# Kernel tuning notes

Hardware: AMD Instinct MI355X
Metric: run time of the kernel (lower is better)

The kernel has to match this reference:

```python
import jax, jax.numpy as jnp
import numpy as np
import math

INPUT_WIDTH = 1024
KEY_WIDTH = 64
VALUE_WIDTH = 64
NUM_HEADS = 16
NUM_GROUPS = 4
HEADS_PER_GROUP = NUM_HEADS // NUM_GROUPS  # w = 4


def setup_inputs() -> dict:
    key = jax.random.key(0)
    k_x, k_q, k_k, k_v, k_p = jax.random.split(key, 5)
    n, s = 2, 2048
    # torch.nn.Linear weights are [out, in]; we store transposed [in, out] for x @ W.
    def lin(k, fan_in, fan_out):
        bound = 1.0 / math.sqrt(fan_in)
        return jax.random.uniform(k, (fan_in, fan_out), minval=-bound, maxval=bound, dtype=jnp.float32)
    return {
        "X": jax.random.normal(k_x, (n, s, INPUT_WIDTH), dtype=jnp.float32),
        "Wq": lin(k_q, INPUT_WIDTH, NUM_HEADS * KEY_WIDTH),
        "Wk": lin(k_k, INPUT_WIDTH, NUM_GROUPS * KEY_WIDTH),
        "Wv": lin(k_v, INPUT_WIDTH, NUM_GROUPS * VALUE_WIDTH),
        "Wpost": lin(k_p, NUM_HEADS * VALUE_WIDTH, INPUT_WIDTH),
    }


def reference(X, Wq, Wk, Wv, Wpost):
    n, s, _ = X.shape
    # Projections (no bias)
    Q = (X @ Wq).reshape(n, s, NUM_GROUPS, HEADS_PER_GROUP, KEY_WIDTH)  # [b,s,g,w,e]
    K = (X @ Wk).reshape(n, s, NUM_GROUPS, KEY_WIDTH)                   # [b,t,g,e]
    V = (X @ Wv).reshape(n, s, NUM_GROUPS, VALUE_WIDTH)                 # [b,t,g,e]
    scale = 1.0 / math.sqrt(KEY_WIDTH)
    # Grouped cross-attention: scores [b,s,t,g,w]
    raw = jnp.einsum('bsgwe,btge->bstgw', Q, K * scale)
    attn = jax.nn.softmax(raw, axis=2)  # softmax over key positions t
    A = jnp.einsum('bstgw,btge->bsgwe', attn, V).reshape(n, s, NUM_HEADS * VALUE_WIDTH)
    P = A @ Wpost
    return X + P
```

## Files before the change

kernel.cpp:

```cpp
#include <hip/hip_runtime.h>
#include <hip/hip_bf16.h>
#include <hip/hip_fp16.h>
#include <math.h>

typedef __attribute__((ext_vector_type(8))) short bfrag8;
typedef __attribute__((ext_vector_type(8))) _Float16 hfrag8;
typedef __attribute__((ext_vector_type(4))) float facc4;
typedef __attribute__((ext_vector_type(16))) float facc16;

#define MFMA16B(a, b, c) __builtin_amdgcn_mfma_f32_16x16x32_bf16((a), (b), (c), 0, 0, 0)
#define MFMA32B(a, b, c) __builtin_amdgcn_mfma_f32_32x32x16_bf16((a), (b), (c), 0, 0, 0)
#define MFMA32H(a, b, c) __builtin_amdgcn_mfma_f32_32x32x16_f16((a), (b), (c), 0, 0, 0)

__device__ __forceinline__ void gload_lds16(const void* g, void* l) {
    __builtin_amdgcn_global_load_lds(
        (const __attribute__((address_space(1))) void*)g,
        (__attribute__((address_space(3))) void*)l, 16, 0, 0);
}

__device__ __forceinline__ unsigned short f2bf(float f) {
    unsigned u = __float_as_uint(f);
    u += 0x7fffu + ((u >> 16) & 1u);
    return (unsigned short)(u >> 16);
}

__device__ __forceinline__ unsigned pk2(float a, float b) {
    auto h = __builtin_amdgcn_cvt_pkrtz(a, b);
    union { decltype(h) h; unsigned u; } c;
    c.h = h;
    return c.u;
}

__device__ __forceinline__ void do_transpose(const float* __restrict__ src,
                                             unsigned short* __restrict__ dst,
                                             int Kdim, int N, int nb, int kb,
                                             float (*tile)[33], int tid) {
    int tx = tid & 31, ty = tid >> 5;
#pragma unroll
    for (int r = ty; r < 32; r += 8)
        tile[r][tx] = src[(size_t)(kb + r) * N + nb + tx];
    __syncthreads();
#pragma unroll
    for (int r = ty; r < 32; r += 8)
        dst[(size_t)(nb + r) * Kdim + kb + tx] = f2bf(tile[tx][r]);
}

__global__ __launch_bounds__(256) void k_prep(
    const float* __restrict__ X, const float* __restrict__ Wq,
    const float* __restrict__ Wk, const float* __restrict__ Wv,
    const float* __restrict__ Wp,
    unsigned short* __restrict__ Xb, unsigned short* __restrict__ Wqkvt,
    unsigned short* __restrict__ Wpt) {
    __shared__ float tile[32][33];
    int blk = blockIdx.x, tid = threadIdx.x;
    if (blk < 4096) {
        int i = (blk * 256 + tid) * 4;
        float4 v = *reinterpret_cast<const float4*>(X + i);
        unsigned short o[4] = {f2bf(v.x), f2bf(v.y), f2bf(v.z), f2bf(v.w)};
        *reinterpret_cast<ulonglong1*>(Xb + i) = *reinterpret_cast<ulonglong1*>(o);
    } else if (blk < 5120) {
        int idx = blk - 4096;
        do_transpose(Wq, Wqkvt, 1024, 1024, (idx & 31) * 32, (idx >> 5) * 32, tile, tid);
    } else if (blk < 5376) {
        int idx = blk - 5120;
        do_transpose(Wk, Wqkvt + 1024 * 1024, 1024, 256, (idx & 7) * 32, (idx >> 3) * 32, tile, tid);
    } else if (blk < 5632) {
        int idx = blk - 5376;
        do_transpose(Wv, Wqkvt + 1280 * 1024, 1024, 256, (idx & 7) * 32, (idx >> 3) * 32, tile, tid);
    } else {
        int idx = blk - 5632;
        do_transpose(Wp, Wpt, 1024, 1024, (idx & 31) * 32, (idx >> 5) * 32, tile, tid);
    }
}

template <int EPI>
__global__ __launch_bounds__(512) void k_gemm_bt(
    const unsigned short* __restrict__ A, const unsigned short* __restrict__ Bt,
    int M, int N, int K,
    unsigned short* __restrict__ Qo, unsigned short* __restrict__ Ko,
    unsigned short* __restrict__ Vto,
    const float* __restrict__ Xres, float* __restrict__ Out) {
    __shared__ char lds[49152];
    const int tid = threadIdx.x;
    const int lane = tid & 63, wid = tid >> 6;
    const int wr = wid >> 1, wc = wid & 1;
    const int l15 = lane & 15, lhi = lane >> 4;
    const int m0 = blockIdx.y * 128, n0 = blockIdx.x * 64;
    const int nk = K >> 6;

    facc4 acc[2][2] = {};

    auto STAGE = [&](int buf, int k0) {
#pragma unroll
        for (int i = 0; i < 2; ++i) {
            int p = (wid * 2 + i) * 1024 + lane * 16;
            int row = p >> 7;
            int src = (p & 127) ^ ((row & 7) << 4);
            gload_lds16(A + (size_t)(m0 + row) * K + k0 + (src >> 1),
                        lds + buf * 16384 + (wid * 2 + i) * 1024);
        }
        {
            int p = wid * 1024 + lane * 16;
            int row = p >> 7;
            int src = (p & 127) ^ ((row & 7) << 4);
            gload_lds16(Bt + (size_t)(n0 + row) * K + k0 + (src >> 1),
                        lds + 32768 + buf * 8192 + wid * 1024);
        }
    };

    STAGE(0, 0);
    __syncthreads();

    for (int t = 0; t < nk; ++t) {
        const int cur = t & 1;
        if (t + 1 < nk) STAGE(cur ^ 1, (t + 1) * 64);
        const char* Ab = lds + cur * 16384;
        const char* Bb = lds + 32768 + cur * 8192;
#pragma unroll
        for (int kc = 0; kc < 2; ++kc) {
            bfrag8 af[2], bfv[2];
#pragma unroll
            for (int mi = 0; mi < 2; ++mi) {
                int row = wr * 32 + mi * 16 + l15;
                int off = (row * 128 + kc * 64 + lhi * 16) ^ ((row & 7) << 4);
                af[mi] = *reinterpret_cast<const bfrag8*>(Ab + off);
            }
#pragma unroll
            for (int ni = 0; ni < 2; ++ni) {
                int row = wc * 32 + ni * 16 + l15;
                int off = (row * 128 + kc * 64 + lhi * 16) ^ ((row & 7) << 4);
                bfv[ni] = *reinterpret_cast<const bfrag8*>(Bb + off);
            }
#pragma unroll
            for (int mi = 0; mi < 2; ++mi)
#pragma unroll
                for (int ni = 0; ni < 2; ++ni)
                    acc[mi][ni] = MFMA16B(af[mi], bfv[ni], acc[mi][ni]);
        }
        __syncthreads();
    }

    if (EPI == 0 && n0 >= 1280) {
        unsigned short* VT = (unsigned short*)lds;
#pragma unroll
        for (int mi = 0; mi < 2; ++mi)
#pragma unroll
            for (int ni = 0; ni < 2; ++ni) {
                int col = wc * 32 + ni * 16 + l15;
                int row0 = wr * 32 + mi * 16 + lhi * 4;
                unsigned long long u = 0;
#pragma unroll
                for (int r = 0; r < 4; ++r)
                    u |= (unsigned long long)__half_as_ushort(__float2half(acc[mi][ni][r]))
                         << (16 * r);
                *reinterpret_cast<unsigned long long*>(VT + col * 136 + row0) = u;
            }
        __syncthreads();
        int c = tid >> 3, part = tid & 7;
        int b = m0 >> 11;
        int g = (n0 - 1280) >> 6;
        unsigned short* dstp =
            Vto + ((size_t)(b * 4 + g) * 64 + c) * 2048 + (m0 & 2047) + part * 16;
        const unsigned short* srcp = VT + c * 136 + part * 16;
        *(reinterpret_cast<uint4*>(dstp) + 0) = *(reinterpret_cast<const uint4*>(srcp) + 0);
        *(reinterpret_cast<uint4*>(dstp) + 1) = *(reinterpret_cast<const uint4*>(srcp) + 1);
        return;
    }

#pragma unroll
    for (int mi = 0; mi < 2; ++mi)
#pragma unroll
        for (int ni = 0; ni < 2; ++ni)
#pragma unroll
            for (int r = 0; r < 4; ++r) {
                int grow = m0 + wr * 32 + mi * 16 + lhi * 4 + r;
                int gcol = n0 + wc * 32 + ni * 16 + l15;
                float v = acc[mi][ni][r];
                if (EPI == 0) {
                    int b = grow >> 11, t = grow & 2047;
                    if (gcol < 1024) {
                        Qo[(size_t)grow * 1024 + gcol] = f2bf(v * 0.18033688f);
                    } else {
                        int cc = gcol - 1024;
                        int g = cc >> 6, e = cc & 63;
                        Ko[(((size_t)(b * 4 + g) * 2048 + t) << 6) + e] = f2bf(v);
                    }
                } else {
                    size_t idx = (size_t)grow * 1024 + gcol;
                    Out[idx] = Xres[idx] + v;
                }
            }
}

__global__ __launch_bounds__(512, 2) void k_attn(
    const unsigned short* __restrict__ Q,
    const unsigned short* __restrict__ Kb,
    const unsigned short* __restrict__ Vt,
    unsigned short* __restrict__ Abuf) {
    __shared__ char smem[49152];

    const int tid = threadIdx.x;
    const int lane = tid & 63, wid = tid >> 6;
    const int kvh = wid >> 2, qw = wid & 3;
    const int l31 = lane & 31, hi = lane >> 5;

    int wg = blockIdx.x;
    int swz = ((wg & 7) << 6) | (wg >> 3);
    const int qt = swz & 15, head = (swz >> 4) & 15, b = swz >> 8;
    const int g = head >> 2;
    const size_t kvK = (size_t)(b * 4 + g) * 2048 * 64;
    const size_t kvV = (size_t)(b * 4 + g) * 64 * 2048;
    const int qrow0 = b * 2048 + qt * 128 + qw * 32;

    bfrag8 qf[4];
#pragma unroll
    for (int ks = 0; ks < 4; ++ks)
        qf[ks] = *reinterpret_cast<const bfrag8*>(
            Q + (size_t)(qrow0 + l31) * 1024 + head * 64 + ks * 16 + hi * 8);

    const int p = qw * 1024 + lane * 16;
    const int rK = p >> 7;
    const int cK = (p & 127) ^ ((rK & 7) << 4);
    const unsigned short* srcK = Kb + kvK + (size_t)(kvh * 1024 + rK) * 64 + (cK >> 1);
    const int rV = p >> 6;
    const int cV = (p & 63) ^ ((rV & 6) << 3);
    const unsigned short* srcV = Vt + kvV + (size_t)rV * 2048 + kvh * 1024 + (cV >> 1);
    const int dK = kvh * 12288 + qw * 1024;
    const int dV = 24576 + kvh * 12288 + qw * 1024;

    facc16 o[2] = {};
    float psA = 0.f, psB = 0.f;

    gload_lds16(srcK, smem + dK);
    gload_lds16(srcV, smem + dV);
    gload_lds16(srcK + 32 * 64, smem + dK + 4096);
    gload_lds16(srcV + 32, smem + dV + 4096);

    for (int t = 0; t < 32; ++t) {
        if (t < 31) asm volatile("s_waitcnt vmcnt(2)" ::: "memory");
        else        asm volatile("s_waitcnt vmcnt(0)" ::: "memory");
        __builtin_amdgcn_s_barrier();
        __builtin_amdgcn_sched_barrier(0);
        if (t < 30) {
            const int bn = (t + 2) % 3;
            gload_lds16(srcK + (size_t)(t + 2) * (32 * 64), smem + dK + bn * 4096);
            gload_lds16(srcV + (size_t)(t + 2) * 32, smem + dV + bn * 4096);
        }
        const char* Kc = smem + kvh * 12288 + (t % 3) * 4096;
        const char* Vc = smem + 24576 + kvh * 12288 + (t % 3) * 4096;

        facc16 s = {};
        __builtin_amdgcn_s_setprio(1);
#pragma unroll
        for (int ks = 0; ks < 4; ++ks) {
            int off = (l31 * 128 + ks * 32 + hi * 16) ^ ((l31 & 7) << 4);
            bfrag8 kf = *reinterpret_cast<const bfrag8*>(Kc + off);
            s = MFMA32B(kf, qf[ks], s);
        }
        __builtin_amdgcn_s_setprio(0);

#pragma unroll
        for (int e = 0; e < 16; e += 2) {
            float e0 = __builtin_amdgcn_exp2f(s[e]);
            float e1 = __builtin_amdgcn_exp2f(s[e + 1]);
            s[e] = e0;
            s[e + 1] = e1;
            psA += e0;
            psB += e1;
        }
#pragma unroll
        for (int kh = 0; kh < 2; ++kh) {
            const int pb = kh * 2;
            unsigned a0 = pk2(s[4 * pb + 0], s[4 * pb + 1]);
            unsigned a1 = pk2(s[4 * pb + 2], s[4 * pb + 3]);
            unsigned b0 = pk2(s[4 * pb + 4], s[4 * pb + 5]);
            unsigned b1 = pk2(s[4 * pb + 6], s[4 * pb + 7]);
            asm("v_permlane32_swap_b32 %0, %1" : "+v"(a0), "+v"(b0));
            asm("v_permlane32_swap_b32 %0, %1" : "+v"(a1), "+v"(b1));
            union { unsigned u[4]; hfrag8 h; } pu;
            pu.u[0] = a0; pu.u[1] = a1; pu.u[2] = b0; pu.u[3] = b1;
            __builtin_amdgcn_s_setprio(1);
#pragma unroll
            for (int ot = 0; ot < 2; ++ot) {
                int row = ot * 32 + l31;
                int off = row * 64 + ((kh * 32 + hi * 16) ^ ((row & 6) << 3));
                hfrag8 vf = *reinterpret_cast<const hfrag8*>(Vc + off);
                o[ot] = MFMA32H(vf, pu.h, o[ot]);
            }
            __builtin_amdgcn_s_setprio(0);
        }
    }
    __syncthreads();

    float psum = psA + psB;
    float* cmO = (float*)smem;
    float* cmL = (float*)(smem + 32768);
    if (kvh == 1) {
#pragma unroll
        for (int ot = 0; ot < 2; ++ot)
#pragma unroll
            for (int r = 0; r < 16; ++r)
                cmO[qw * 2048 + (ot * 16 + r) * 64 + lane] = o[ot][r];
        cmL[qw * 64 + lane] = psum;
    }
    __syncthreads();
    if (kvh == 0) {
#pragma unroll
        for (int ot = 0; ot < 2; ++ot)
#pragma unroll
            for (int r = 0; r < 16; ++r)
                o[ot][r] += cmO[qw * 2048 + (ot * 16 + r) * 64 + lane];
        psum += cmL[qw * 64 + lane];

        float l = psum + __shfl_xor(psum, 32, 64);
        float rl = 1.0f / l;
        int arow = qrow0 + l31;
#pragma unroll
        for (int ot = 0; ot < 2; ++ot)
#pragma unroll
            for (int p2 = 0; p2 < 4; ++p2) {
                unsigned long long u = 0;
#pragma unroll
                for (int r = 0; r < 4; ++r)
                    u |= (unsigned long long)f2bf(o[ot][4 * p2 + r] * rl) << (16 * r);
                *reinterpret_cast<unsigned long long*>(
                    Abuf + (size_t)arow * 1024 + head * 64 + ot * 32 + p2 * 8 + hi * 4) = u;
            }
    }
}


extern "C" void kernel_launch(void* const* d_in, const int* in_sizes, int n_in,
                              void* d_out, int out_size, void* d_ws, size_t ws_size,
                              hipStream_t stream) {
    const float* X = (const float*)d_in[0];
    const float* Wq = (const float*)d_in[1];
    const float* Wk = (const float*)d_in[2];
    const float* Wv = (const float*)d_in[3];
    const float* Wpost = (const float*)d_in[4];
    float* Out = (float*)d_out;

    unsigned short* Xb = (unsigned short*)d_ws;
    unsigned short* Wqkvt = Xb + 4096 * 1024;
    unsigned short* Wpt = Wqkvt + 1536 * 1024;
    unsigned short* Qb = Wpt + 1024 * 1024;
    unsigned short* Kbuf = Qb + 4096 * 1024;
    unsigned short* Vtbuf = Kbuf + 8 * 2048 * 64;
    unsigned short* Abuf = Vtbuf + 8 * 2048 * 64;

    k_prep<<<6656, 256, 0, stream>>>(X, Wq, Wk, Wv, Wpost, Xb, Wqkvt, Wpt);

    k_gemm_bt<0><<<dim3(24, 32), 512, 0, stream>>>(Xb, Wqkvt, 4096, 1536, 1024,
                                                   Qb, Kbuf, Vtbuf, nullptr, nullptr);

    k_attn<<<512, 512, 0, stream>>>(Qb, Kbuf, Vtbuf, Abuf);

    k_gemm_bt<1><<<dim3(16, 32), 512, 0, stream>>>(Abuf, Wpt, 4096, 1024, 1024,
                                                   nullptr, nullptr, nullptr, X, Out);
}
```

Before: 89.43 us.

## Load V in 64-key tiles with double buffering and 128B swizzled rows

V^T tiles are now fetched as 64-key chunks (128-byte rows) every other iteration into a double buffer, instead of 32-key chunks each iteration in a triple buffer. K keeps its triple-buffered per-iteration pipeline, and the waitcnt values alternate to match the uneven issue pattern. The aim is longer contiguous global reads and fewer V load instructions. In exchange, LDS use grows and the prefetch distance for V changes. The QK accumulator is also initialised from a zero register rather than a fresh zero vector.

```diff
diff --git a/kernel.cpp b/kernel.cpp
--- a/kernel.cpp
+++ b/kernel.cpp
@@ -197,7 +197,7 @@
     const unsigned short* __restrict__ Kb,
     const unsigned short* __restrict__ Vt,
     unsigned short* __restrict__ Abuf) {
-    __shared__ char smem[49152];
+    __shared__ char smem[57344];
 
     const int tid = threadIdx.x;
     const int lane = tid & 63, wid = tid >> 6;
@@ -218,44 +218,58 @@
         qf[ks] = *reinterpret_cast<const bfrag8*>(
             Q + (size_t)(qrow0 + l31) * 1024 + head * 64 + ks * 16 + hi * 8);
 
-    const int p = qw * 1024 + lane * 16;
-    const int rK = p >> 7;
-    const int cK = (p & 127) ^ ((rK & 7) << 4);
-    const unsigned short* srcK = Kb + kvK + (size_t)(kvh * 1024 + rK) * 64 + (cK >> 1);
-    const int rV = p >> 6;
-    const int cV = (p & 63) ^ ((rV & 6) << 3);
-    const unsigned short* srcV = Vt + kvV + (size_t)rV * 2048 + kvh * 1024 + (cV >> 1);
+    const int pK = qw * 1024 + lane * 16;
+    const int rK = pK >> 7;
+    const int cKb = (pK & 127) ^ ((rK & 7) << 4);
+    const unsigned short* srcK = Kb + kvK + (size_t)(kvh * 1024 + rK) * 64 + (cKb >> 1);
     const int dK = kvh * 12288 + qw * 1024;
-    const int dV = 24576 + kvh * 12288 + qw * 1024;
+
+    const unsigned short* srcV[2];
+#pragma unroll
+    for (int j = 0; j < 2; ++j) {
+        int p = qw * 2048 + j * 1024 + lane * 16;
+        int rV = p >> 7;
+        int cVb = (p & 127) ^ ((rV & 7) << 4);
+        srcV[j] = Vt + kvV + (size_t)rV * 2048 + kvh * 1024 + (cVb >> 1);
+    }
+    const int dV0 = 24576 + kvh * 16384 + qw * 2048;
 
     facc16 o[2] = {};
+    facc16 fz = {};
     float psA = 0.f, psB = 0.f;
 
     gload_lds16(srcK, smem + dK);
-    gload_lds16(srcV, smem + dV);
+    gload_lds16(srcV[0], smem + dV0);
+    gload_lds16(srcV[1], smem + dV0 + 1024);
     gload_lds16(srcK + 32 * 64, smem + dK + 4096);
-    gload_lds16(srcV + 32, smem + dV + 4096);
 
     for (int t = 0; t < 32; ++t) {
-        if (t < 31) asm volatile("s_waitcnt vmcnt(2)" ::: "memory");
-        else        asm volatile("s_waitcnt vmcnt(0)" ::: "memory");
+        if (t == 31)      asm volatile("s_waitcnt vmcnt(0)" ::: "memory");
+        else if (t & 1)   asm volatile("s_waitcnt vmcnt(3)" ::: "memory");
+        else              asm volatile("s_waitcnt vmcnt(1)" ::: "memory");
         __builtin_amdgcn_s_barrier();
         __builtin_amdgcn_sched_barrier(0);
         if (t < 30) {
-            const int bn = (t + 2) % 3;
-            gload_lds16(srcK + (size_t)(t + 2) * (32 * 64), smem + dK + bn * 4096);
-            gload_lds16(srcV + (size_t)(t + 2) * 32, smem + dV + bn * 4096);
+            gload_lds16(srcK + (size_t)(t + 2) * (32 * 64),
+                        smem + dK + ((t + 2) % 3) * 4096);
+            if (!(t & 1)) {
+                int tv = (t >> 1) + 1;
+                int vb = (tv & 1) * 8192;
+                gload_lds16(srcV[0] + (size_t)tv * 64, smem + dV0 + vb);
+                gload_lds16(srcV[1] + (size_t)tv * 64, smem + dV0 + vb + 1024);
+            }
         }
         const char* Kc = smem + kvh * 12288 + (t % 3) * 4096;
-        const char* Vc = smem + 24576 + kvh * 12288 + (t % 3) * 4096;
-
-        facc16 s = {};
+        const char* Vc = smem + 24576 + kvh * 16384 + ((t >> 1) & 1) * 8192;
+        const int vcol = (t & 1) * 64;
+
+        facc16 s;
         __builtin_amdgcn_s_setprio(1);
 #pragma unroll
         for (int ks = 0; ks < 4; ++ks) {
             int off = (l31 * 128 + ks * 32 + hi * 16) ^ ((l31 & 7) << 4);
             bfrag8 kf = *reinterpret_cast<const bfrag8*>(Kc + off);
-            s = MFMA32B(kf, qf[ks], s);
+            s = MFMA32B(kf, qf[ks], ks == 0 ? fz : s);
         }
         __builtin_amdgcn_s_setprio(0);
 
@@ -283,8 +297,8 @@
 #pragma unroll
             for (int ot = 0; ot < 2; ++ot) {
                 int row = ot * 32 + l31;
-                int off = row * 64 + ((kh * 32 + hi * 16) ^ ((row & 6) << 3));
-                hfrag8 vf = *reinterpret_cast<const hfrag8*>(Vc + off);
+                int colb = (vcol + kh * 32 + hi * 16) ^ ((row & 7) << 4);
+                hfrag8 vf = *reinterpret_cast<const hfrag8*>(Vc + row * 128 + colb);
                 o[ot] = MFMA32H(vf, pu.h, o[ot]);
             }
             __builtin_amdgcn_s_setprio(0);
```

Result: no change. 90.75 us (+1.5%).

## Software-pipeline QK^T one tile ahead and use 4-stage LDS ring

Applied to the files above, without the earlier changes.

Computes the score MFMA for the next key tile before the exp/PV work of the current tile, so the exp2 VALU work can overlap with matrix-core work. The K/V LDS ring grows from 3 to 4 stages (48KB to 64KB shared memory), and prefetch loads are now issued before the barrier. The larger LDS footprint with launch bounds (512,2) may limit occupancy, and the extra live accumulator raises register pressure.

```diff
diff --git a/kernel.cpp b/kernel.cpp
--- a/kernel.cpp
+++ b/kernel.cpp
@@ -197,7 +197,7 @@
     const unsigned short* __restrict__ Kb,
     const unsigned short* __restrict__ Vt,
     unsigned short* __restrict__ Abuf) {
-    __shared__ char smem[49152];
+    __shared__ char smem[65536];
 
     const int tid = threadIdx.x;
     const int lane = tid & 63, wid = tid >> 6;
@@ -225,56 +225,73 @@
     const int rV = p >> 6;
     const int cV = (p & 63) ^ ((rV & 6) << 3);
     const unsigned short* srcV = Vt + kvV + (size_t)rV * 2048 + kvh * 1024 + (cV >> 1);
-    const int dK = kvh * 12288 + qw * 1024;
-    const int dV = 24576 + kvh * 12288 + qw * 1024;
+    const int dK = kvh * 16384 + qw * 1024;
+    const int dV = 32768 + kvh * 16384 + qw * 1024;
 
     facc16 o[2] = {};
+    const facc16 fz = {};
     float psA = 0.f, psB = 0.f;
 
     gload_lds16(srcK, smem + dK);
     gload_lds16(srcV, smem + dV);
     gload_lds16(srcK + 32 * 64, smem + dK + 4096);
     gload_lds16(srcV + 32, smem + dV + 4096);
+    asm volatile("s_waitcnt vmcnt(2)" ::: "memory");
+    __builtin_amdgcn_s_barrier();
+
+    facc16 scur;
+    {
+        const char* K0 = smem + kvh * 16384;
+#pragma unroll
+        for (int ks = 0; ks < 4; ++ks) {
+            int off = (l31 * 128 + ks * 32 + hi * 16) ^ ((l31 & 7) << 4);
+            bfrag8 kf = *reinterpret_cast<const bfrag8*>(K0 + off);
+            scur = MFMA32B(kf, qf[ks], ks == 0 ? fz : scur);
+        }
+    }
 
     for (int t = 0; t < 32; ++t) {
-        if (t < 31) asm volatile("s_waitcnt vmcnt(2)" ::: "memory");
-        else        asm volatile("s_waitcnt vmcnt(0)" ::: "memory");
+        if (t < 30) {
+            const int bn = (t + 2) & 3;
+            gload_lds16(srcK + (size_t)(t + 2) * (32 * 64), smem + dK + bn * 4096);
+            gload_lds16(srcV + (size_t)(t + 2) * 32, smem + dV + bn * 4096);
+            asm volatile("s_waitcnt vmcnt(2)" ::: "memory");
+        } else {
+            asm volatile("s_waitcnt vmcnt(0)" ::: "memory");
+        }
         __builtin_amdgcn_s_barrier();
         __builtin_amdgcn_sched_barrier(0);
-        if (t < 30) {
-            const int bn = (t + 2) % 3;
-            gload_lds16(srcK + (size_t)(t + 2) * (32 * 64), smem + dK + bn * 4096);
-            gload_lds16(srcV + (size_t)(t + 2) * 32, smem + dV + bn * 4096);
-        }
-        const char* Kc = smem + kvh * 12288 + (t % 3) * 4096;
-        const char* Vc = smem + 24576 + kvh * 12288 + (t % 3) * 4096;
-
-        facc16 s = {};
-        __builtin_amdgcn_s_setprio(1);
-#pragma unroll
-        for (int ks = 0; ks < 4; ++ks) {
-            int off = (l31 * 128 + ks * 32 + hi * 16) ^ ((l31 & 7) << 4);
-            bfrag8 kf = *reinterpret_cast<const bfrag8*>(Kc + off);
-            s = MFMA32B(kf, qf[ks], s);
-        }
-        __builtin_amdgcn_s_setprio(0);
-
+
+        facc16 snxt;
+        if (t < 31) {
+            const char* Kn = smem + kvh * 16384 + ((t + 1) & 3) * 4096;
+            __builtin_amdgcn_s_setprio(1);
+#pragma unroll
+            for (int ks = 0; ks < 4; ++ks) {
+                int off = (l31 * 128 + ks * 32 + hi * 16) ^ ((l31 & 7) << 4);
+                bfrag8 kf = *reinterpret_cast<const bfrag8*>(Kn + off);
+                snxt = MFMA32B(kf, qf[ks], ks == 0 ? fz : snxt);
+            }
+            __builtin_amdgcn_s_setprio(0);
+        }
+
+        const char* Vc = smem + 32768 + kvh * 16384 + (t & 3) * 4096;
 #pragma unroll
         for (int e = 0; e < 16; e += 2) {
-            float e0 = __builtin_amdgcn_exp2f(s[e]);
-            float e1 = __builtin_amdgcn_exp2f(s[e + 1]);
-            s[e] = e0;
-            s[e + 1] = e1;
+            float e0 = __builtin_amdgcn_exp2f(scur[e]);
+            float e1 = __builtin_amdgcn_exp2f(scur[e + 1]);
+            scur[e] = e0;
+            scur[e + 1] = e1;
             psA += e0;
             psB += e1;
         }
 #pragma unroll
         for (int kh = 0; kh < 2; ++kh) {
             const int pb = kh * 2;
-            unsigned a0 = pk2(s[4 * pb + 0], s[4 * pb + 1]);
-            unsigned a1 = pk2(s[4 * pb + 2], s[4 * pb + 3]);
-            unsigned b0 = pk2(s[4 * pb + 4], s[4 * pb + 5]);
-            unsigned b1 = pk2(s[4 * pb + 6], s[4 * pb + 7]);
+            unsigned a0 = pk2(scur[4 * pb + 0], scur[4 * pb + 1]);
+            unsigned a1 = pk2(scur[4 * pb + 2], scur[4 * pb + 3]);
+            unsigned b0 = pk2(scur[4 * pb + 4], scur[4 * pb + 5]);
+            unsigned b1 = pk2(scur[4 * pb + 6], scur[4 * pb + 7]);
             asm("v_permlane32_swap_b32 %0, %1" : "+v"(a0), "+v"(b0));
             asm("v_permlane32_swap_b32 %0, %1" : "+v"(a1), "+v"(b1));
             union { unsigned u[4]; hfrag8 h; } pu;
@@ -289,6 +306,7 @@
             }
             __builtin_amdgcn_s_setprio(0);
         }
+        scur = snxt;
     }
     __syncthreads();
 
```

Result: no change. 89.92 us (+0.6%).

## Load attention K/V fragments directly from global into registers, drop LDS staging

Applied to the files above, without the earlier changes.

The attention kernel no longer stages K and V tiles through LDS with async global-to-LDS loads and barriers. Each wave now reads its MFMA fragments straight from global memory, prefetching the next K tile one iteration ahead. Workgroups shrink from 512 to 256 threads (64 query rows instead of 128), with twice as many blocks. This removes the per-iteration barrier and LDS traffic, but K/V reuse across query waves now depends on L1/L2 caching, so global load traffic per wave goes up and V loads are not prefetched.

```diff
diff --git a/kernel.cpp b/kernel.cpp
--- a/kernel.cpp
+++ b/kernel.cpp
@@ -192,25 +192,25 @@
             }
 }
 
-__global__ __launch_bounds__(512, 2) void k_attn(
+__global__ __launch_bounds__(256, 3) void k_attn(
     const unsigned short* __restrict__ Q,
     const unsigned short* __restrict__ Kb,
     const unsigned short* __restrict__ Vt,
     unsigned short* __restrict__ Abuf) {
-    __shared__ char smem[49152];
+    __shared__ float cm[2][2112 + 64];
 
     const int tid = threadIdx.x;
     const int lane = tid & 63, wid = tid >> 6;
-    const int kvh = wid >> 2, qw = wid & 3;
+    const int kvh = wid >> 1, qw = wid & 1;
     const int l31 = lane & 31, hi = lane >> 5;
 
     int wg = blockIdx.x;
-    int swz = ((wg & 7) << 6) | (wg >> 3);
-    const int qt = swz & 15, head = (swz >> 4) & 15, b = swz >> 8;
+    int swz = ((wg & 7) << 7) | (wg >> 3);
+    const int qt = swz & 31, head = (swz >> 5) & 15, b = swz >> 9;
     const int g = head >> 2;
     const size_t kvK = (size_t)(b * 4 + g) * 2048 * 64;
     const size_t kvV = (size_t)(b * 4 + g) * 64 * 2048;
-    const int qrow0 = b * 2048 + qt * 128 + qw * 32;
+    const int qrow0 = b * 2048 + qt * 64 + qw * 32;
 
     bfrag8 qf[4];
 #pragma unroll
@@ -218,45 +218,40 @@
         qf[ks] = *reinterpret_cast<const bfrag8*>(
             Q + (size_t)(qrow0 + l31) * 1024 + head * 64 + ks * 16 + hi * 8);
 
-    const int p = qw * 1024 + lane * 16;
-    const int rK = p >> 7;
-    const int cK = (p & 127) ^ ((rK & 7) << 4);
-    const unsigned short* srcK = Kb + kvK + (size_t)(kvh * 1024 + rK) * 64 + (cK >> 1);
-    const int rV = p >> 6;
-    const int cV = (p & 63) ^ ((rV & 6) << 3);
-    const unsigned short* srcV = Vt + kvV + (size_t)rV * 2048 + kvh * 1024 + (cV >> 1);
-    const int dK = kvh * 12288 + qw * 1024;
-    const int dV = 24576 + kvh * 12288 + qw * 1024;
+    const unsigned short* Kp =
+        Kb + kvK + ((size_t)(kvh * 1024 + l31)) * 64 + hi * 8;
+    const unsigned short* Vp =
+        Vt + kvV + (size_t)l31 * 2048 + kvh * 1024 + hi * 8;
 
     facc16 o[2] = {};
+    const facc16 fz = {};
     float psA = 0.f, psB = 0.f;
 
-    gload_lds16(srcK, smem + dK);
-    gload_lds16(srcV, smem + dV);
-    gload_lds16(srcK + 32 * 64, smem + dK + 4096);
-    gload_lds16(srcV + 32, smem + dV + 4096);
+    bfrag8 kfC[4], kfN[4];
+#pragma unroll
+    for (int ks = 0; ks < 4; ++ks)
+        kfC[ks] = *reinterpret_cast<const bfrag8*>(Kp + ks * 16);
 
     for (int t = 0; t < 32; ++t) {
-        if (t < 31) asm volatile("s_waitcnt vmcnt(2)" ::: "memory");
-        else        asm volatile("s_waitcnt vmcnt(0)" ::: "memory");
-        __builtin_amdgcn_s_barrier();
-        __builtin_amdgcn_sched_barrier(0);
-        if (t < 30) {
-            const int bn = (t + 2) % 3;
-            gload_lds16(srcK + (size_t)(t + 2) * (32 * 64), smem + dK + bn * 4096);
-            gload_lds16(srcV + (size_t)(t + 2) * 32, smem + dV + bn * 4096);
-        }
-        const char* Kc = smem + kvh * 12288 + (t % 3) * 4096;
-        const char* Vc = smem + 24576 + kvh * 12288 + (t % 3) * 4096;
-
-        facc16 s = {};
+        if (t < 31) {
+            const unsigned short* kp1 = Kp + (size_t)(t + 1) * 2048;
+#pragma unroll
+            for (int ks = 0; ks < 4; ++ks)
+                kfN[ks] = *reinterpret_cast<const bfrag8*>(kp1 + ks * 16);
+        }
+        hfrag8 vf[2][2];
+#pragma unroll
+        for (int kh = 0; kh < 2; ++kh)
+#pragma unroll
+            for (int ot = 0; ot < 2; ++ot)
+                vf[kh][ot] = *reinterpret_cast<const hfrag8*>(
+                    Vp + (size_t)(ot * 32) * 2048 + t * 32 + kh * 16);
+
+        facc16 s;
         __builtin_amdgcn_s_setprio(1);
 #pragma unroll
-        for (int ks = 0; ks < 4; ++ks) {
-            int off = (l31 * 128 + ks * 32 + hi * 16) ^ ((l31 & 7) << 4);
-            bfrag8 kf = *reinterpret_cast<const bfrag8*>(Kc + off);
-            s = MFMA32B(kf, qf[ks], s);
-        }
+        for (int ks = 0; ks < 4; ++ks)
+            s = MFMA32B(kfC[ks], qf[ks], ks == 0 ? fz : s);
         __builtin_amdgcn_s_setprio(0);
 
 #pragma unroll
@@ -281,27 +276,23 @@
             pu.u[0] = a0; pu.u[1] = a1; pu.u[2] = b0; pu.u[3] = b1;
             __builtin_amdgcn_s_setprio(1);
 #pragma unroll
-            for (int ot = 0; ot < 2; ++ot) {
-                int row = ot * 32 + l31;
-                int off = row * 64 + ((kh * 32 + hi * 16) ^ ((row & 6) << 3));
-                hfrag8 vf = *reinterpret_cast<const hfrag8*>(Vc + off);
-                o[ot] = MFMA32H(vf, pu.h, o[ot]);
-            }
+            for (int ot = 0; ot < 2; ++ot)
+                o[ot] = MFMA32H(vf[kh][ot], pu.h, o[ot]);
             __builtin_amdgcn_s_setprio(0);
         }
-    }
+#pragma unroll
+        for (int ks = 0; ks < 4; ++ks) kfC[ks] = kfN[ks];
+    }
+
+    float psum = psA + psB;
     __syncthreads();
-
-    float psum = psA + psB;
-    float* cmO = (float*)smem;
-    float* cmL = (float*)(smem + 32768);
     if (kvh == 1) {
 #pragma unroll
         for (int ot = 0; ot < 2; ++ot)
 #pragma unroll
             for (int r = 0; r < 16; ++r)
-                cmO[qw * 2048 + (ot * 16 + r) * 64 + lane] = o[ot][r];
-        cmL[qw * 64 + lane] = psum;
+                cm[qw][(ot * 16 + r) * 64 + lane] = o[ot][r];
+        cm[qw][2048 + lane] = psum;
     }
     __syncthreads();
     if (kvh == 0) {
@@ -309,8 +300,8 @@
         for (int ot = 0; ot < 2; ++ot)
 #pragma unroll
             for (int r = 0; r < 16; ++r)
-                o[ot][r] += cmO[qw * 2048 + (ot * 16 + r) * 64 + lane];
-        psum += cmL[qw * 64 + lane];
+                o[ot][r] += cm[qw][(ot * 16 + r) * 64 + lane];
+        psum += cm[qw][2048 + lane];
 
         float l = psum + __shfl_xor(psum, 32, 64);
         float rl = 1.0f / l;
@@ -353,7 +344,7 @@
     k_gemm_bt<0><<<dim3(24, 32), 512, 0, stream>>>(Xb, Wqkvt, 4096, 1536, 1024,
                                                    Qb, Kbuf, Vtbuf, nullptr, nullptr);
 
-    k_attn<<<512, 512, 0, stream>>>(Qb, Kbuf, Vtbuf, Abuf);
+    k_attn<<<1024, 256, 0, stream>>>(Qb, Kbuf, Vtbuf, Abuf);
 
     k_gemm_bt<1><<<dim3(16, 32), 512, 0, stream>>>(Abuf, Wpt, 4096, 1024, 1024,
                                                    nullptr, nullptr, nullptr, X, Out);
```

New measurement: 164.1 us. +83.5%, slower.
